# Optimization experiments

Measured on AMD Instinct MI355X. Metric: run time of the kernel, lower is better.

The kernel has to match this reference:

```python
import jax, jax.numpy as jnp
import numpy as np

EPS = 1e-5


def _cbr(z, W, bn, relu=True):
    # z: [b, Cin, L]; W: [Cout, Cin]; bn: [4, Cout] = (gamma, beta, mean, var)
    # 1x1 Conv2d (bias=False) over a [b, Cin, L, 1] tensor == channel matmul.
    y = jnp.einsum('oi,bil->bol', W, z)
    g, b_, m, v = bn[0], bn[1], bn[2], bn[3]
    y = g[:, None] * (y - m[:, None]) * jax.lax.rsqrt(v[:, None] + EPS) + b_[:, None]
    return jax.nn.relu(y) if relu else y


def setup_inputs() -> dict:
    key = jax.random.key(0)
    ks = jax.random.split(key, 13)
    b, c, h, w = 32, 512, 48, 48
    in_spatial = h * w          # 2304
    inter_spatial = in_spatial // 4  # 576
    inter_channel = c // 4      # 128
    ncc = 1 + inter_channel     # 129
    return {
        'x': jax.random.normal(ks[0], (b, c, h, w), jnp.float32),
        'W_theta': jax.random.normal(ks[1], (inter_spatial, in_spatial), jnp.float32) * 0.02,
        'bn_theta': jax.random.uniform(ks[2], (4, inter_spatial), jnp.float32),
        'W_phi': jax.random.normal(ks[3], (inter_spatial, in_spatial), jnp.float32) * 0.02,
        'bn_phi': jax.random.uniform(ks[4], (4, inter_spatial), jnp.float32),
        'W_gx': jax.random.normal(ks[5], (inter_spatial, in_spatial), jnp.float32) * 0.02,
        'bn_gx': jax.random.uniform(ks[6], (4, inter_spatial), jnp.float32),
        'W_gg': jax.random.normal(ks[7], (inter_channel, 2 * c), jnp.float32) * 0.02,
        'bn_gg': jax.random.uniform(ks[8], (4, inter_channel), jnp.float32),
        'W_c1': jax.random.normal(ks[9], (ncc // 2, ncc), jnp.float32) * 0.02,
        'bn_c1': jax.random.uniform(ks[10], (4, ncc // 2), jnp.float32),
        'W_c2': jax.random.normal(ks[11], (1, ncc // 2), jnp.float32) * 0.02,
        'bn_c2': jax.random.uniform(ks[12], (4, 1), jnp.float32),
    }


def reference(x, W_theta, bn_theta, W_phi, bn_phi, W_gx, bn_gx,
              W_gg, bn_gg, W_c1, bn_c1, W_c2, bn_c2):
    b, c, h, w = x.shape
    xc = x.reshape(b, c, h * w).transpose(0, 2, 1)          # [b, hw, c]
    xc1 = _cbr(xc, W_theta, bn_theta).transpose(0, 2, 1)    # [b, c, is]
    xc2 = _cbr(xc, W_phi, bn_phi)                           # [b, is, c]
    Gc = jnp.einsum('bcs,bsd->bcd', xc1, xc2)               # [b, c, c]
    Gc_joint = jnp.concatenate([Gc.transpose(0, 2, 1), Gc], axis=1)  # [b, 2c, c]
    Gc_joint = _cbr(Gc_joint, W_gg, bn_gg)                  # [b, ic, c]
    g_xc = _cbr(xc, W_gx, bn_gx).mean(axis=1, keepdims=True)  # [b, 1, c]
    yc = jnp.concatenate([g_xc, Gc_joint], axis=1)          # [b, 1+ic, c]
    wy = _cbr(yc, W_c1, bn_c1)
    wy = _cbr(wy, W_c2, bn_c2, relu=False)                  # [b, 1, c]
    gate = jax.nn.sigmoid(wy)[:, 0, :, None, None]          # [b, c, 1, 1]
    return gate * x + x
```

## Files before the change

kernel.cpp:

```cpp
#include <hip/hip_runtime.h>
#include <cstdint>

#define EPSV 1e-5f
typedef unsigned short u16;
typedef __attribute__((ext_vector_type(8))) short bh8;
typedef __attribute__((ext_vector_type(4))) float f4;

__device__ __forceinline__ float bf2f(u16 h) { return __uint_as_float((unsigned)h << 16); }
__device__ __forceinline__ u16 f2bf(float x) {
    unsigned u = __float_as_uint(x);
    u += 0x7fffu + ((u >> 16) & 1u);
    return (u16)(u >> 16);
}

__device__ __forceinline__ void gl16(const void* g, const void* s) {
    __builtin_amdgcn_global_load_lds(
        reinterpret_cast<const __attribute__((address_space(1))) void*>((uintptr_t)g),
        reinterpret_cast<__attribute__((address_space(3))) void*>((unsigned)(uintptr_t)s),
        16, 0, 0);
}

__device__ __forceinline__ void core2(
    const u16* __restrict__ Ah, const u16* __restrict__ Al,
    const u16* __restrict__ Bh, const u16* __restrict__ Bl,
    long ldA, long ldB, int K, int rowA0, int rowB0,
    u16* lds, f4 acc[4][4])
{
    const int tid = threadIdx.x, l = tid & 63, w = tid >> 6;
    const int wr = w >> 1, wc = w & 1;
    const int srow = tid >> 2;
    const int schunk = ((tid & 3) ^ ((tid >> 3) & 3)) << 3;
    const size_t aoff = (size_t)(rowA0 + srow) * ldA + schunk;
    const size_t boff = (size_t)(rowB0 + srow) * ldB + schunk;
    const size_t a64 = (size_t)64 * ldA, b64 = (size_t)64 * ldB;
    const int rr = l & 15, cq = l >> 4;
    const int roff = rr * 64 + (((cq ^ ((rr >> 1) & 3))) << 4);
    char* const base0 = (char*)lds;
    char* const base1 = (char*)lds + 32768;
    const int nt = K >> 5;

#define STAGE_SWZ(base, s0) do { \
    gl16(Ah + aoff + (s0),       (base) +         w * 1024); \
    gl16(Ah + aoff + a64 + (s0), (base) +  4096 + w * 1024); \
    gl16(Al + aoff + (s0),       (base) +  8192 + w * 1024); \
    gl16(Al + aoff + a64 + (s0), (base) + 12288 + w * 1024); \
    gl16(Bh + boff + (s0),       (base) + 16384 + w * 1024); \
    gl16(Bh + boff + b64 + (s0), (base) + 20480 + w * 1024); \
    gl16(Bl + boff + (s0),       (base) + 24576 + w * 1024); \
    gl16(Bl + boff + b64 + (s0), (base) + 28672 + w * 1024); \
} while (0)

    STAGE_SWZ(base0, 0);
    __syncthreads();
    int p = 0;
    for (int t = 0; t < nt; ++t) {
        if (t + 1 < nt) STAGE_SWZ(p ? base0 : base1, (size_t)(t + 1) << 5);
        const char* buf = p ? base1 : base0;
        bh8 a_h[4], a_l[4], b_h[4], b_l[4];
#pragma unroll
        for (int i = 0; i < 4; ++i) {
            a_h[i] = *(const bh8*)(buf + (wr * 4 + i) * 1024 + roff);
            a_l[i] = *(const bh8*)(buf + 8192 + (wr * 4 + i) * 1024 + roff);
            b_h[i] = *(const bh8*)(buf + 16384 + (wc * 4 + i) * 1024 + roff);
            b_l[i] = *(const bh8*)(buf + 24576 + (wc * 4 + i) * 1024 + roff);
        }
#pragma unroll
        for (int i = 0; i < 4; ++i)
#pragma unroll
            for (int j = 0; j < 4; ++j)
                acc[i][j] = __builtin_amdgcn_mfma_f32_16x16x32_bf16(a_h[i], b_h[j], acc[i][j], 0, 0, 0);
#pragma unroll
        for (int i = 0; i < 4; ++i)
#pragma unroll
            for (int j = 0; j < 4; ++j)
                acc[i][j] = __builtin_amdgcn_mfma_f32_16x16x32_bf16(a_h[i], b_l[j], acc[i][j], 0, 0, 0);
#pragma unroll
        for (int i = 0; i < 4; ++i)
#pragma unroll
            for (int j = 0; j < 4; ++j)
                acc[i][j] = __builtin_amdgcn_mfma_f32_16x16x32_bf16(a_l[i], b_h[j], acc[i][j], 0, 0, 0);
        __syncthreads();
        p ^= 1;
    }
#undef STAGE_SWZ
}

__global__ __launch_bounds__(512) void gemm_s1_v6b(
    const u16* __restrict__ Xh, const u16* __restrict__ Xl,
    const u16* __restrict__ W0h, const u16* __restrict__ W0l,
    const u16* __restrict__ W1h, const u16* __restrict__ W1l,
    const u16* __restrict__ W2h, const u16* __restrict__ W2l,
    const float* __restrict__ bn0, const float* __restrict__ bn1,
    const float* __restrict__ bn2,
    float* __restrict__ gxc_part,
    u16* __restrict__ Y1h, u16* __restrict__ Y1l,
    u16* __restrict__ Y2h, u16* __restrict__ Y2l)
{
    const int h = blockIdx.x;
    const int orig = (h & 7) * 120 + (h >> 3);
    const int ow = orig % 15;
    const int rest = orig / 15;
    const int ct = rest & 1, bz = rest >> 1;
    const int wi = ow / 5, otw = ow % 5;
    const bool full = (wi != 0);

    const u16* Bh = wi == 0 ? W0h : wi == 1 ? W1h : W2h;
    const u16* Bl = wi == 0 ? W0l : wi == 1 ? W1l : W2l;
    const float* bnp = wi == 0 ? bn0 : wi == 1 ? bn1 : bn2;
    u16* Yh = wi == 1 ? Y1h : Y2h;
    u16* Yl = wi == 1 ? Y1l : Y2l;

    __shared__ u16 lds[73728];

    const int tid = threadIdx.x, l = tid & 63, w = tid >> 6;
    const int wm = w >> 1, wn = w & 1;
    const long ldK = 2304;
    const int rowA0 = bz * 512 + ct * 256;
    const int rowB0 = otw * 128;
    const int srow = tid >> 2;
    const int schunk = ((tid & 3) ^ ((tid >> 3) & 3)) << 3;
    const size_t aoff = (size_t)(rowA0 + srow) * ldK + schunk;
    const size_t boff = (size_t)(rowB0 + srow) * ldK + schunk;
    const size_t a128 = (size_t)128 * ldK;
    const int rr = l & 15, cq2 = l >> 4;
    const int roff = rr * 64 + ((cq2 ^ ((rr >> 1) & 3)) << 4);
    char* const ldsb = (char*)lds;
    const int nt = 72;

#define ST_AHI(sb, s0) do { \
    gl16(Xh + aoff + (s0),        (sb) +         w * 1024); \
    gl16(Xh + aoff + a128 + (s0), (sb) +  8192 + w * 1024); } while (0)
#define ST_ALO(sb, s0) do { \
    gl16(Xl + aoff + (s0),        (sb) + 16384 + w * 1024); \
    gl16(Xl + aoff + a128 + (s0), (sb) + 24576 + w * 1024); } while (0)
#define ST_BHI(sb, s0) gl16(Bh + boff + (s0), (sb) + 32768 + w * 1024)
#define ST_BLO(sb, s0) gl16(Bl + boff + (s0), (sb) + 40960 + w * 1024)

    f4 acc[4][4];
    const f4 z4 = {0.f, 0.f, 0.f, 0.f};
#pragma unroll
    for (int i = 0; i < 4; ++i)
#pragma unroll
        for (int j = 0; j < 4; ++j) acc[i][j] = z4;

    ST_AHI(ldsb, 0); if (full) ST_ALO(ldsb, 0); ST_BHI(ldsb, 0); ST_BLO(ldsb, 0);
    ST_AHI(ldsb + 49152, 32); if (full) ST_ALO(ldsb + 49152, 32);
    ST_BHI(ldsb + 49152, 32); ST_BLO(ldsb + 49152, 32);
    if (full) asm volatile("s_waitcnt vmcnt(6)" ::: "memory");
    else      asm volatile("s_waitcnt vmcnt(4)" ::: "memory");
    __builtin_amdgcn_sched_barrier(0);
    __builtin_amdgcn_s_barrier();

    for (int t = 0; t < nt; ++t) {
        const char* buf = ldsb + (t % 3) * 49152;
        char* sbuf = ldsb + ((t + 2) % 3) * 49152;
        const bool pre = (t + 2 < nt);
        const int s0 = (t + 2) << 5;

        bh8 a_h[4], b_h[4], a_l[4], b_l[4];
#pragma unroll
        for (int i = 0; i < 4; ++i)
            a_h[i] = *(const bh8*)(buf + (wm * 4 + i) * 1024 + roff);
#pragma unroll
        for (int j = 0; j < 4; ++j)
            b_h[j] = *(const bh8*)(buf + 32768 + (wn * 4 + j) * 1024 + roff);
        if (pre) ST_AHI(sbuf, s0);
        __builtin_amdgcn_s_barrier();
        __builtin_amdgcn_s_setprio(1);
#pragma unroll
        for (int i = 0; i < 4; ++i)
#pragma unroll
            for (int j = 0; j < 4; ++j)
                acc[i][j] = __builtin_amdgcn_mfma_f32_16x16x32_bf16(a_h[i], b_h[j], acc[i][j], 0, 0, 0);
        __builtin_amdgcn_s_setprio(0);
        __builtin_amdgcn_s_barrier();
        if (full) {
#pragma unroll
            for (int i = 0; i < 4; ++i)
                a_l[i] = *(const bh8*)(buf + 16384 + (wm * 4 + i) * 1024 + roff);
        }
#pragma unroll
        for (int j = 0; j < 4; ++j)
            b_l[j] = *(const bh8*)(buf + 40960 + (wn * 4 + j) * 1024 + roff);
        if (pre) { if (full) ST_ALO(sbuf, s0); ST_BHI(sbuf, s0); }
        __builtin_amdgcn_s_barrier();
        __builtin_amdgcn_s_setprio(1);
#pragma unroll
        for (int i = 0; i < 4; ++i)
#pragma unroll
            for (int j = 0; j < 4; ++j)
                acc[i][j] = __builtin_amdgcn_mfma_f32_16x16x32_bf16(a_h[i], b_l[j], acc[i][j], 0, 0, 0);
        __builtin_amdgcn_s_setprio(0);
        __builtin_amdgcn_s_barrier();
        if (pre) ST_BLO(sbuf, s0);
        if (t + 1 < nt) {
            if (pre) {
                if (full) asm volatile("s_waitcnt vmcnt(6)" ::: "memory");
                else      asm volatile("s_waitcnt vmcnt(4)" ::: "memory");
            } else {
                asm volatile("s_waitcnt vmcnt(0)" ::: "memory");
            }
            __builtin_amdgcn_sched_barrier(0);
        }
        __builtin_amdgcn_s_barrier();
        if (full) {
            __builtin_amdgcn_s_setprio(1);
#pragma unroll
            for (int i = 0; i < 4; ++i)
#pragma unroll
                for (int j = 0; j < 4; ++j)
                    acc[i][j] = __builtin_amdgcn_mfma_f32_16x16x32_bf16(a_l[i], b_h[j], acc[i][j], 0, 0, 0);
            __builtin_amdgcn_s_setprio(0);
        }
        __builtin_amdgcn_s_barrier();
    }
#undef ST_AHI
#undef ST_ALO
#undef ST_BHI
#undef ST_BLO

    const int mb = ct * 256 + wm * 64;
    const int nbw = otw * 128 + wn * 64;
    const int lm = l & 15, cq = l >> 4;

    if (wi == 0) {
        float rs[4][4] = {};
#pragma unroll
        for (int j = 0; j < 4; ++j) {
            const int o = nbw + j * 16 + lm;
            const bool val = (o < 576);
            float sc = 0.f, sh = 0.f;
            if (val) {
                const float gg = bnp[o], be = bnp[576 + o], mm = bnp[1152 + o], vv = bnp[1728 + o];
                sc = gg * rsqrtf(vv + EPSV);
                sh = be - mm * sc;
            }
#pragma unroll
            for (int i = 0; i < 4; ++i)
#pragma unroll
                for (int r = 0; r < 4; ++r)
                    rs[i][r] += val ? fmaxf(acc[i][j][r] * sc + sh, 0.f) : 0.f;
        }
        __syncthreads();
        float* ldsF = (float*)lds;
#pragma unroll
        for (int i = 0; i < 4; ++i)
#pragma unroll
            for (int r = 0; r < 4; ++r) {
                float v = rs[i][r];
                v += __shfl_xor(v, 1, 64);
                v += __shfl_xor(v, 2, 64);
                v += __shfl_xor(v, 4, 64);
                v += __shfl_xor(v, 8, 64);
                if (lm == 0)
                    ldsF[wn * 256 + wm * 64 + i * 16 + cq * 4 + r] = v;
            }
        __syncthreads();
        if (tid < 256)
            gxc_part[(size_t)otw * 16384 + (size_t)bz * 512 + ct * 256 + tid]
                = ldsF[tid] + ldsF[256 + tid];
    } else {
#pragma unroll
        for (int j = 0; j < 4; ++j) {
            const int o = nbw + j * 16 + lm;
            const bool val = (o < 576);
            float sc = 0.f, sh = 0.f;
            if (val) {
                const float gg = bnp[o], be = bnp[576 + o], mm = bnp[1152 + o], vv = bnp[1728 + o];
                sc = gg * rsqrtf(vv + EPSV);
                sh = be - mm * sc;
            }
#pragma unroll
            for (int i = 0; i < 4; ++i) {
                const int c = mb + i * 16 + (cq << 2);
#pragma unroll
                for (int r = 0; r < 4; ++r) {
                    const float y = val ? fmaxf(acc[i][j][r] * sc + sh, 0.f) : 0.f;
                    const u16 hh = f2bf(y);
                    const u16 lo = f2bf(y - bf2f(hh));
                    const size_t off = ((size_t)bz * 512 + c + r) * 640 + o;
                    Yh[off] = hh; Yl[off] = lo;
                }
            }
        }
    }
}

__global__ __launch_bounds__(256) void gemm_u(
    const u16* __restrict__ Wggh, const u16* __restrict__ Wggl,
    const u16* __restrict__ tnth, const u16* __restrict__ tntl,
    const u16* __restrict__ pnth, const u16* __restrict__ pntl,
    u16* __restrict__ U1h, u16* __restrict__ U1l,
    u16* __restrict__ U2h, u16* __restrict__ U2l)
{
    const int h = blockIdx.x;
    const int orig = (h & 7) * 40 + (h >> 3);
    const int ot = orig % 5;
    const int rest = orig / 5;
    const int u = rest & 1, b = rest >> 1;

    const u16* Ah = Wggh + (u ? 512 : 0);
    const u16* Al = Wggl + (u ? 512 : 0);
    const u16* Bh = u ? tnth : pnth;
    const u16* Bl = u ? tntl : pntl;

    __shared__ u16 lds[32768];
    f4 acc[4][4];
    const f4 z4 = {0.f, 0.f, 0.f, 0.f};
#pragma unroll
    for (int i = 0; i < 4; ++i)
#pragma unroll
        for (int j = 0; j < 4; ++j) acc[i][j] = z4;

    core2(Ah, Al, Bh, Bl, 1024, 512, 512, 0, b * 640 + ot * 128, lds, acc);

    u16* Uh = u ? U2h : U1h;
    u16* Ul = u ? U2l : U1l;
    const int l = threadIdx.x & 63, w = threadIdx.x >> 6;
    const int wr = w >> 1, wc = w & 1;
#pragma unroll
    for (int i = 0; i < 4; ++i)
#pragma unroll
        for (int j = 0; j < 4; ++j)
#pragma unroll
            for (int r = 0; r < 4; ++r) {
                const int irow = wr * 64 + i * 16 + ((l >> 4) << 2) + r;
                const int ocol = ot * 128 + wc * 64 + j * 16 + (l & 15);
                const float v = acc[i][j][r];
                const u16 hh = f2bf(v);
                const u16 lo = f2bf(v - bf2f(hh));
                const size_t off = ((size_t)b * 128 + irow) * 640 + ocol;
                Uh[off] = hh; Ul[off] = lo;
            }
}

__global__ __launch_bounds__(256) void gemm_term_p(
    const u16* __restrict__ U1h, const u16* __restrict__ U1l,
    const u16* __restrict__ U2h, const u16* __restrict__ U2l,
    const u16* __restrict__ tth, const u16* __restrict__ ttl,
    const u16* __restrict__ pth, const u16* __restrict__ ptl,
    float* __restrict__ GGa, float* __restrict__ GGb)
{
    const int h = blockIdx.x;
    const int orig = (h & 7) * 32 + (h >> 3);
    const int dt = orig & 3;
    const int u = (orig >> 2) & 1;
    const int b = orig >> 3;

    const u16* Ah = u ? U2h : U1h;
    const u16* Al = u ? U2l : U1l;
    const u16* Bh = u ? pth : tth;
    const u16* Bl = u ? ptl : ttl;
    float* G = u ? GGb : GGa;

    __shared__ u16 lds[32768];
    f4 acc[4][4];
    const f4 z4 = {0.f, 0.f, 0.f, 0.f};
#pragma unroll
    for (int i = 0; i < 4; ++i)
#pragma unroll
        for (int j = 0; j < 4; ++j) acc[i][j] = z4;

    core2(Ah, Al, Bh, Bl, 640, 640, 640,
          b * 128, b * 512 + dt * 128, lds, acc);

    const int l = threadIdx.x & 63, w = threadIdx.x >> 6;
    const int wr = w >> 1, wc = w & 1;
#pragma unroll
    for (int i = 0; i < 4; ++i)
#pragma unroll
        for (int j = 0; j < 4; ++j)
#pragma unroll
            for (int r = 0; r < 4; ++r) {
                const int irow = wr * 64 + i * 16 + ((l >> 4) << 2) + r;
                const int dcol = dt * 128 + wc * 64 + j * 16 + (l & 15);
                G[((size_t)b * 128 + irow) * 512 + dcol] = acc[i][j][r];
            }
}

__global__ __launch_bounds__(256) void transpose_y(
    const u16* __restrict__ s0, u16* __restrict__ d0,
    const u16* __restrict__ s1, u16* __restrict__ d1,
    const u16* __restrict__ s2, u16* __restrict__ d2,
    const u16* __restrict__ s3, u16* __restrict__ d3)
{
    const int pz = blockIdx.z;
    const int b = pz >> 2, pl = pz & 3;
    const u16* src = pl == 0 ? s0 : pl == 1 ? s1 : pl == 2 ? s2 : s3;
    u16* dst = pl == 0 ? d0 : pl == 1 ? d1 : pl == 2 ? d2 : d3;
    const int o0 = blockIdx.x * 64, c0 = blockIdx.y * 64;
    __shared__ u16 t[64][72];
    const int tid = threadIdx.x;
#pragma unroll
    for (int rdx = tid; rdx < 512; rdx += 256) {
        const int c = rdx >> 3, oc = (rdx & 7) << 3;
        *(bh8*)&t[c][oc] = *(const bh8*)&src[((size_t)b * 512 + c0 + c) * 640 + o0 + oc];
    }
    __syncthreads();
#pragma unroll
    for (int wdx = tid; wdx < 512; wdx += 256) {
        const int o = wdx >> 3, cc = (wdx & 7) << 3;
        u16 v[8];
#pragma unroll
        for (int e = 0; e < 8; ++e) v[e] = t[cc + e][o];
        *(bh8*)&dst[((size_t)b * 640 + o0 + o) * 512 + c0 + cc] = *(bh8*)&v[0];
    }
}

__global__ __launch_bounds__(256) void conv_split(
    const float* __restrict__ in, u16* __restrict__ hi, u16* __restrict__ lo, long n8)
{
    long i = (long)blockIdx.x * 256 + threadIdx.x;
    const long stride = (long)gridDim.x * 256;
    for (; i < n8; i += stride) {
        const float4 a = ((const float4*)in)[2 * i];
        const float4 b = ((const float4*)in)[2 * i + 1];
        const float v[8] = {a.x, a.y, a.z, a.w, b.x, b.y, b.z, b.w};
        unsigned hw[4], lw[4];
#pragma unroll
        for (int k = 0; k < 4; ++k) {
            const u16 h0 = f2bf(v[2 * k]), h1 = f2bf(v[2 * k + 1]);
            const u16 l0 = f2bf(v[2 * k] - bf2f(h0)), l1 = f2bf(v[2 * k + 1] - bf2f(h1));
            hw[k] = (unsigned)h0 | ((unsigned)h1 << 16);
            lw[k] = (unsigned)l0 | ((unsigned)l1 << 16);
        }
        *(uint4*)&hi[8 * i] = make_uint4(hw[0], hw[1], hw[2], hw[3]);
        *(uint4*)&lo[8 * i] = make_uint4(lw[0], lw[1], lw[2], lw[3]);
    }
}

__global__ __launch_bounds__(256) void conv_w_pad3(
    const float* __restrict__ Wg, const float* __restrict__ Wt,
    const float* __restrict__ Wp,
    u16* __restrict__ Hg, u16* __restrict__ Lg,
    u16* __restrict__ Ht, u16* __restrict__ Lt,
    u16* __restrict__ Hp, u16* __restrict__ Lp,
    int rows, long n8)
{
    const int wsel = blockIdx.y;
    const float* W = wsel == 0 ? Wg : wsel == 1 ? Wt : Wp;
    u16* hi = wsel == 0 ? Hg : wsel == 1 ? Ht : Hp;
    u16* lo = wsel == 0 ? Lg : wsel == 1 ? Lt : Lp;

    const long i = (long)blockIdx.x * 256 + threadIdx.x;
    if (i >= n8) return;
    const long e = i * 8;
    const int row = (int)(e / 2304);
    unsigned hw[4] = {0, 0, 0, 0}, lw[4] = {0, 0, 0, 0};
    if (row < rows) {
        const float4 a = ((const float4*)W)[2 * i];
        const float4 b = ((const float4*)W)[2 * i + 1];
        const float v[8] = {a.x, a.y, a.z, a.w, b.x, b.y, b.z, b.w};
#pragma unroll
        for (int k = 0; k < 4; ++k) {
            const u16 h0 = f2bf(v[2 * k]), h1 = f2bf(v[2 * k + 1]);
            const u16 l0 = f2bf(v[2 * k] - bf2f(h0)), l1 = f2bf(v[2 * k + 1] - bf2f(h1));
            hw[k] = (unsigned)h0 | ((unsigned)h1 << 16);
            lw[k] = (unsigned)l0 | ((unsigned)l1 << 16);
        }
    }
    *(uint4*)&hi[8 * i] = make_uint4(hw[0], hw[1], hw[2], hw[3]);
    *(uint4*)&lo[8 * i] = make_uint4(lw[0], lw[1], lw[2], lw[3]);
}

__global__ __launch_bounds__(256)
void gate_kernel(const float* __restrict__ gxp,
                 const float* __restrict__ GGa, const float* __restrict__ GGb,
                 const float* __restrict__ bngg,
                 const float* __restrict__ Wc1, const float* __restrict__ bn1,
                 const float* __restrict__ Wc2, const float* __restrict__ bn2,
                 float* __restrict__ gate, int IC, int D, int OC)
{
    const int b  = blockIdx.y;
    const int d0 = blockIdx.x * 64;

    __shared__ float yc_s[129][64];
    __shared__ float part[4][64];

    const int tid = threadIdx.x;
    for (int idx = tid; idx < 129 * 64; idx += 256) {
        const int j = idx >> 6, d = idx & 63;
        float v;
        if (j == 0) {
            float s = 0.f;
#pragma unroll
            for (int t = 0; t < 5; ++t)
                s += gxp[(size_t)t * 16384 + (size_t)b * 512 + d0 + d];
            v = s * (1.f / 576.f);
        } else {
            const int i = j - 1;
            const float g = bngg[i], be = bngg[128 + i];
            const float m = bngg[256 + i], vv = bngg[384 + i];
            const float sc = g * rsqrtf(vv + EPSV);
            const float sh = be - m * sc;
            const size_t o = ((size_t)b * IC + i) * D + d0 + d;
            v = fmaxf((GGa[o] + GGb[o]) * sc + sh, 0.f);
        }
        yc_s[j][d] = v;
    }
    __syncthreads();

    const int d = tid & 63;
    const int q = tid >> 6;
    float acc2 = 0.f;
    for (int o = q * 16; o < q * 16 + 16; ++o) {
        float s = 0.f;
        const float* __restrict__ w = &Wc1[o * 129];
        for (int j = 0; j < 129; ++j) s = fmaf(w[j], yc_s[j][d], s);
        const float g1 = bn1[o], be1 = bn1[OC + o], m1 = bn1[2 * OC + o], v1 = bn1[3 * OC + o];
        const float sc = g1 / sqrtf(v1 + EPSV);
        const float w1 = fmaxf(s * sc + (be1 - m1 * sc), 0.f);
        acc2 = fmaf(Wc2[o], w1, acc2);
    }
    part[q][d] = acc2;
    __syncthreads();
    if (q == 0) {
        const float s = part[0][d] + part[1][d] + part[2][d] + part[3][d];
        const float g2 = bn2[0], be2 = bn2[1], m2 = bn2[2], v2 = bn2[3];
        const float sc = g2 / sqrtf(v2 + EPSV);
        const float wy = s * sc + (be2 - m2 * sc);
        gate[b * D + d0 + d] = 1.f / (1.f + expf(-wy));
    }
}

__global__ __launch_bounds__(256)
void final_kernel(const float* __restrict__ x, const float* __restrict__ gate,
                  float* __restrict__ out, long n4, int sp4)
{
    long i = (long)blockIdx.x * blockDim.x + threadIdx.x;
    const long stride = (long)gridDim.x * blockDim.x;
    for (; i < n4; i += stride) {
        float4 v = ((const float4*)x)[i];
        const long bc = i / sp4;
        const float gm = 1.f + gate[bc];
        v.x *= gm; v.y *= gm; v.z *= gm; v.w *= gm;
        ((float4*)out)[i] = v;
    }
}

extern "C" void kernel_launch(void* const* d_in, const int* in_sizes, int n_in,
                              void* d_out, int out_size, void* d_ws, size_t ws_size,
                              hipStream_t stream)
{
    const float* x        = (const float*)d_in[0];
    const float* W_theta  = (const float*)d_in[1];
    const float* bn_theta = (const float*)d_in[2];
    const float* W_phi    = (const float*)d_in[3];
    const float* bn_phi   = (const float*)d_in[4];
    const float* W_gx     = (const float*)d_in[5];
    const float* bn_gx    = (const float*)d_in[6];
    const float* W_gg     = (const float*)d_in[7];
    const float* bn_gg    = (const float*)d_in[8];
    const float* W_c1     = (const float*)d_in[9];
    const float* bn_c1    = (const float*)d_in[10];
    const float* W_c2     = (const float*)d_in[11];
    const float* bn_c2    = (const float*)d_in[12];
    float* out = (float*)d_out;

    const int B = 32, C = 512, S = 2304, O = 576, OP = 640, IC = 128, OC = 64;
    const size_t P  = (size_t)B * C * OP;
    const size_t WP = (size_t)OP * S;
    const size_t UP = (size_t)B * IC * OP;

    u16* tth = (u16*)d_out;
    u16* ttl = tth + P;
    u16* pth = ttl + P;
    u16* ptl = pth + P;
    u16* Wgh = ptl + P;
    u16* Wgl = Wgh + WP;
    u16* Wth = Wgl + WP;
    u16* Wtl = Wth + WP;
    u16* Wph = Wtl + WP;
    u16* Wpl = Wph + WP;
    u16* wggh = Wpl + WP;
    u16* wggl = wggh + (size_t)IC * 1024;
    u16* u1h = wggl + (size_t)IC * 1024;
    u16* u1l = u1h + UP;
    u16* u2h = u1l + UP;
    u16* u2l = u2h + UP;
    float* GGa = (float*)(u2l + UP);
    float* GGb = GGa + (size_t)B * IC * C;

    u16* Xhi  = (u16*)d_ws;
    u16* Xlo  = Xhi + (size_t)B * C * S;
    u16* tnth = (u16*)d_ws;
    u16* tntl = tnth + P;
    u16* pnth = tntl + P;
    u16* pntl = pnth + P;
    float* gxc_part = (float*)(Xlo + (size_t)B * C * S);
    float* gate = gxc_part + (size_t)5 * B * C;

    const dim3 blk(256);

    const long wN8 = (long)WP / 8;
    conv_w_pad3<<<dim3((unsigned)(wN8 / 256), 3), blk, 0, stream>>>(
        W_gx, W_theta, W_phi, Wgh, Wgl, Wth, Wtl, Wph, Wpl, O, wN8);
    conv_split<<<dim3(64), blk, 0, stream>>>(W_gg, wggh, wggl, (long)IC * 1024 / 8);

    conv_split<<<dim3(2048), blk, 0, stream>>>(x, Xhi, Xlo, (long)B * C * S / 8);
    gemm_s1_v6b<<<dim3(960), dim3(512), 0, stream>>>(
        Xhi, Xlo, Wgh, Wgl, Wth, Wtl, Wph, Wpl,
        bn_gx, bn_theta, bn_phi,
        gxc_part, tth, ttl, pth, ptl);

    transpose_y<<<dim3(10, 8, 128), blk, 0, stream>>>(
        tth, tnth, ttl, tntl, pth, pnth, ptl, pntl);

    gemm_u<<<dim3(320), blk, 0, stream>>>(wggh, wggl, tnth, tntl, pnth, pntl,
                                          u1h, u1l, u2h, u2l);

    gemm_term_p<<<dim3(256), blk, 0, stream>>>(u1h, u1l, u2h, u2l,
                                               tth, ttl, pth, ptl, GGa, GGb);

    gate_kernel<<<dim3(C / 64, B), blk, 0, stream>>>(
        gxc_part, GGa, GGb, bn_gg, W_c1, bn_c1, W_c2, bn_c2,
        gate, IC, C, OC);

    final_kernel<<<dim3(2048), blk, 0, stream>>>(x, gate, out,
                                                 (long)B * C * S / 4, S / 4);
}
```

Measured before the change: 611.1 us.

## Restructure stage-1 GEMM main loop into single-barrier issue-all-then-compute pipeline

The stage-1 GEMM loop used to interleave four separate global-to-LDS prefetch groups with four barrier-separated MFMA phases per K step. Now all prefetches for step t+2 are issued at the top of the iteration, followed by one vmcnt wait and one barrier. All LDS fragment reads then run together and the three MFMA groups execute back to back under raised priority, with an lgkmcnt wait and barrier at the end. This cuts per-iteration barriers from five to two and gives the scheduler longer MFMA runs. In exchange, more registers are live at once and loads are no longer spread evenly between compute phases.

After: 653.8 us. 1.07x slower.

```diff
diff --git a/kernel.cpp b/kernel.cpp
--- a/kernel.cpp
+++ b/kernel.cpp
@@ -85,7 +85,7 @@
 #undef STAGE_SWZ
 }
 
-__global__ __launch_bounds__(512) void gemm_s1_v6b(
+__global__ __launch_bounds__(512) void gemm_s1_v9(
     const u16* __restrict__ Xh, const u16* __restrict__ Xl,
     const u16* __restrict__ W0h, const u16* __restrict__ W0l,
     const u16* __restrict__ W1h, const u16* __restrict__ W1l,
@@ -127,14 +127,16 @@
     char* const ldsb = (char*)lds;
     const int nt = 72;
 
-#define ST_AHI(sb, s0) do { \
+#define ST_ALL(sb, s0) do { \
     gl16(Xh + aoff + (s0),        (sb) +         w * 1024); \
-    gl16(Xh + aoff + a128 + (s0), (sb) +  8192 + w * 1024); } while (0)
-#define ST_ALO(sb, s0) do { \
-    gl16(Xl + aoff + (s0),        (sb) + 16384 + w * 1024); \
-    gl16(Xl + aoff + a128 + (s0), (sb) + 24576 + w * 1024); } while (0)
-#define ST_BHI(sb, s0) gl16(Bh + boff + (s0), (sb) + 32768 + w * 1024)
-#define ST_BLO(sb, s0) gl16(Bl + boff + (s0), (sb) + 40960 + w * 1024)
+    gl16(Xh + aoff + a128 + (s0), (sb) +  8192 + w * 1024); \
+    if (full) { \
+        gl16(Xl + aoff + (s0),        (sb) + 16384 + w * 1024); \
+        gl16(Xl + aoff + a128 + (s0), (sb) + 24576 + w * 1024); \
+    } \
+    gl16(Bh + boff + (s0), (sb) + 32768 + w * 1024); \
+    gl16(Bl + boff + (s0), (sb) + 40960 + w * 1024); \
+} while (0)
 
     f4 acc[4][4];
     const f4 z4 = {0.f, 0.f, 0.f, 0.f};
@@ -143,81 +145,66 @@
 #pragma unroll
         for (int j = 0; j < 4; ++j) acc[i][j] = z4;
 
-    ST_AHI(ldsb, 0); if (full) ST_ALO(ldsb, 0); ST_BHI(ldsb, 0); ST_BLO(ldsb, 0);
-    ST_AHI(ldsb + 49152, 32); if (full) ST_ALO(ldsb + 49152, 32);
-    ST_BHI(ldsb + 49152, 32); ST_BLO(ldsb + 49152, 32);
-    if (full) asm volatile("s_waitcnt vmcnt(6)" ::: "memory");
-    else      asm volatile("s_waitcnt vmcnt(4)" ::: "memory");
-    __builtin_amdgcn_sched_barrier(0);
-    __builtin_amdgcn_s_barrier();
+    ST_ALL(ldsb, 0);
+    ST_ALL(ldsb + 49152, 32);
 
     for (int t = 0; t < nt; ++t) {
         const char* buf = ldsb + (t % 3) * 49152;
         char* sbuf = ldsb + ((t + 2) % 3) * 49152;
         const bool pre = (t + 2 < nt);
-        const int s0 = (t + 2) << 5;
-
+
+        if (pre) ST_ALL(sbuf, (t + 2) << 5);
+        if (pre) {
+            if (full) asm volatile("s_waitcnt vmcnt(12)" ::: "memory");
+            else      asm volatile("s_waitcnt vmcnt(8)"  ::: "memory");
+        } else if (t + 1 < nt) {
+            if (full) asm volatile("s_waitcnt vmcnt(6)" ::: "memory");
+            else      asm volatile("s_waitcnt vmcnt(4)" ::: "memory");
+        } else {
+            asm volatile("s_waitcnt vmcnt(0)" ::: "memory");
+        }
+        __builtin_amdgcn_sched_barrier(0);
+        __builtin_amdgcn_s_barrier();
+
+        __builtin_amdgcn_s_setprio(1);
         bh8 a_h[4], b_h[4], a_l[4], b_l[4];
 #pragma unroll
         for (int i = 0; i < 4; ++i)
             a_h[i] = *(const bh8*)(buf + (wm * 4 + i) * 1024 + roff);
 #pragma unroll
-        for (int j = 0; j < 4; ++j)
+        for (int j = 0; j < 4; ++j) {
             b_h[j] = *(const bh8*)(buf + 32768 + (wn * 4 + j) * 1024 + roff);
-        if (pre) ST_AHI(sbuf, s0);
-        __builtin_amdgcn_s_barrier();
-        __builtin_amdgcn_s_setprio(1);
+            b_l[j] = *(const bh8*)(buf + 40960 + (wn * 4 + j) * 1024 + roff);
+        }
+        if (full) {
+#pragma unroll
+            for (int i = 0; i < 4; ++i)
+                a_l[i] = *(const bh8*)(buf + 16384 + (wm * 4 + i) * 1024 + roff);
+        }
 #pragma unroll
         for (int i = 0; i < 4; ++i)
 #pragma unroll
             for (int j = 0; j < 4; ++j)
                 acc[i][j] = __builtin_amdgcn_mfma_f32_16x16x32_bf16(a_h[i], b_h[j], acc[i][j], 0, 0, 0);
-        __builtin_amdgcn_s_setprio(0);
-        __builtin_amdgcn_s_barrier();
-        if (full) {
-#pragma unroll
-            for (int i = 0; i < 4; ++i)
-                a_l[i] = *(const bh8*)(buf + 16384 + (wm * 4 + i) * 1024 + roff);
-        }
-#pragma unroll
-        for (int j = 0; j < 4; ++j)
-            b_l[j] = *(const bh8*)(buf + 40960 + (wn * 4 + j) * 1024 + roff);
-        if (pre) { if (full) ST_ALO(sbuf, s0); ST_BHI(sbuf, s0); }
-        __builtin_amdgcn_s_barrier();
-        __builtin_amdgcn_s_setprio(1);
 #pragma unroll
         for (int i = 0; i < 4; ++i)
 #pragma unroll
             for (int j = 0; j < 4; ++j)
                 acc[i][j] = __builtin_amdgcn_mfma_f32_16x16x32_bf16(a_h[i], b_l[j], acc[i][j], 0, 0, 0);
-        __builtin_amdgcn_s_setprio(0);
-        __builtin_amdgcn_s_barrier();
-        if (pre) ST_BLO(sbuf, s0);
-        if (t + 1 < nt) {
-            if (pre) {
-                if (full) asm volatile("s_waitcnt vmcnt(6)" ::: "memory");
-                else      asm volatile("s_waitcnt vmcnt(4)" ::: "memory");
-            } else {
-                asm volatile("s_waitcnt vmcnt(0)" ::: "memory");
-            }
-            __builtin_amdgcn_sched_barrier(0);
-        }
-        __builtin_amdgcn_s_barrier();
         if (full) {
-            __builtin_amdgcn_s_setprio(1);
 #pragma unroll
             for (int i = 0; i < 4; ++i)
 #pragma unroll
                 for (int j = 0; j < 4; ++j)
                     acc[i][j] = __builtin_amdgcn_mfma_f32_16x16x32_bf16(a_l[i], b_h[j], acc[i][j], 0, 0, 0);
-            __builtin_amdgcn_s_setprio(0);
-        }
+        }
+        __builtin_amdgcn_s_setprio(0);
+
+        asm volatile("s_waitcnt lgkmcnt(0)" ::: "memory");
+        __builtin_amdgcn_sched_barrier(0);
         __builtin_amdgcn_s_barrier();
     }
-#undef ST_AHI
-#undef ST_ALO
-#undef ST_BHI
-#undef ST_BLO
+#undef ST_ALL
 
     const int mb = ct * 256 + wm * 64;
     const int nbw = otw * 128 + wn * 64;
@@ -598,7 +585,7 @@
     conv_split<<<dim3(64), blk, 0, stream>>>(W_gg, wggh, wggl, (long)IC * 1024 / 8);
 
     conv_split<<<dim3(2048), blk, 0, stream>>>(x, Xhi, Xlo, (long)B * C * S / 8);
-    gemm_s1_v6b<<<dim3(960), dim3(512), 0, stream>>>(
+    gemm_s1_v9<<<dim3(960), dim3(512), 0, stream>>>(
         Xhi, Xlo, Wgh, Wgl, Wth, Wtl, Wph, Wpl,
         bn_gx, bn_theta, bn_phi,
         gxc_part, tth, ttl, pth, ptl);
```
